# Kernel tuning notes

Hardware: AMD Instinct MI355X
Metric: run time of the kernel (lower is better)

Reference implementation:

```python
import jax, jax.numpy as jnp
import numpy as np

B, CIN, COUT, H, W = 4, 4, 8, 256, 256
FFTH, FFTW = 2 * H - 1, 2 * W - 1  # fftsize = insize + outsize - 1 (padding=True, stride=1)


def setup_inputs() -> dict:
    key = jax.random.key(0)
    k_im, k_w, k_b = jax.random.split(key, 3)
    im = jax.random.normal(k_im, (B, CIN, H, W), dtype=jnp.float32)
    # learned frequency-domain kernel, last dim = (real, imag)
    weight = jax.random.normal(k_w, (COUT, CIN, FFTH, FFTW, 2), dtype=jnp.float32)
    bias = jax.random.normal(k_b, (COUT, 1, 1), dtype=jnp.float32)
    return {"im": im, "weight": weight, "bias": bias}


def reference(im, weight, bias):
    b, cin, h, w = im.shape
    ffth, fftw = 2 * h - 1, 2 * w - 1
    # zero-pad spatially to fftsize; imaginary part is zero (torch pads a trailing complex dim)
    im_p = jnp.pad(im, ((0, 0), (0, 0), (0, ffth - h), (0, fftw - w)))
    f_im = jnp.fft.fft2(im_p.astype(jnp.complex64))              # [B, Cin, fftH, fftW]
    wc = jax.lax.complex(weight[..., 0], weight[..., 1])         # [O, Cin, fftH, fftW]
    # broadcast complex multiply + in-channel reduction fused as a per-frequency contraction;
    # ifft is linear so summing over in-channels before ifft matches the original math
    feats = jnp.einsum('bchw,ochw->bohw', f_im, wc)              # [B, O, fftH, fftW]
    real = jnp.fft.ifft2(feats).real                             # real_feats_mode='index' -> real part
    # crop: cropsize = fftsize - insize = (H-1, W-1); left = floor/2, right = ceil/2
    cl_h, cr_h = (h - 1) // 2, h // 2
    cl_w, cr_w = (w - 1) // 2, w // 2
    real = real[:, :, cl_h:ffth - cr_h, cl_w:fftw - cr_w]        # [B, O, H, W]
    return real + bias                                           # bias [O,1,1] broadcasts
```

## Files before the change

### kernel.cpp

```cpp
#include <hip/hip_runtime.h>
#include <math.h>

#define NN 511
#define HH 256
#define BB 4
#define CINC 4
#define COUTC 8
#define CROP 127
#define INV_NN2 (1.0f / ((float)NN * (float)NN))

typedef _Float16 f16;
typedef _Float16 f16x8 __attribute__((ext_vector_type(8)));
typedef float    f32x4 __attribute__((ext_vector_type(4)));

__device__ __forceinline__ void twid(int a, int b, float& c, float& s) {
    int m = (a * b) % NN;
    float phi = (float)(2.0 * M_PI / (double)NN) * (float)m;
    __sincosf(phi, &s, &c);
}

__global__ void prep_all(const float* __restrict__ im,
                         f16* __restrict__ Aa, f16* __restrict__ Bb,
                         f16* __restrict__ Bd, f16* __restrict__ Ae,
                         f16* __restrict__ imT, f16* __restrict__ feats) {
    int idx = blockIdx.x * 256 + threadIdx.x;
    if (idx < 131072) {
        int m = idx >> 8, y = idx & 255;
        float c, s;
        if (m < 256) { twid(m, y, c, s);       Aa[idx] = (f16)c;    }
        else         { twid(m - 256, y, c, s); Aa[idx] = (f16)(-s); }
    } else if (idx < 655360) {
        int i = idx - 131072;
        int n = i >> 9, k = i & 511;
        float v = 0.f;
        if (n < 2 * NN) {
            int vv = (n < NN) ? n : n - NN;
            int x  = k & 255;
            float c, s; twid(vv, x, c, s);
            if (n < NN) v = (k < 256) ? c : s;
            else        v = (k < 256) ? -s : c;
        }
        Bb[i] = (f16)v;
    } else if (idx < 1179648) {
        int i = idx - 655360;
        int n = i >> 10, k = i & 1023;
        float v = 0.f;
        if (k < 2 * NN) {
            int x  = n & 255;
            int vv = (k < NN) ? k : k - NN;
            float c, s; twid(vv, x + CROP, c, s);
            if (n < 256) v = (k < NN) ? c : -s;
            else         v = (k < NN) ? s : c;
        }
        Bd[i] = (f16)v;
    } else if (idx < 1310720) {
        int i = idx - 1179648;
        int y = i >> 9, k = i & 511;
        float c, s;
        if (k < 256) { twid(k, y + CROP, c, s);       Ae[i] = (f16)c;    }
        else         { twid(k - 256, y + CROP, c, s); Ae[i] = (f16)(-s); }
    } else if (idx < 2359296) {
        int i = idx - 1310720;
        int bc = i >> 16, r = i & 65535;
        int y = r >> 8, x = r & 255;
        imT[(size_t)bc * 65536 + x * 256 + y] = (f16)im[i];
    } else if (idx < 2375680) {
        int i = idx - 2359296;
        feats[(size_t)(i >> 1) * 1024 + 1022 + (i & 1)] = (f16)0.f;
    }
}

__global__ void cmul_h(const f16* __restrict__ F, const float2* __restrict__ W,
                       f16* __restrict__ feats) {
    int idx = blockIdx.x * 256 + threadIdx.x;
    if (idx >= 256 * NN) return;
    int u = idx / NN, v = idx - u * NN;
    int u2 = (u == 0) ? 0 : NN - u;
    int v2 = (v == 0) ? 0 : NN - v;
    float fr[BB][CINC], fi[BB][CINC];
    #pragma unroll
    for (int b = 0; b < BB; ++b)
        #pragma unroll
        for (int c = 0; c < CINC; ++c) {
            size_t row = ((size_t)((b * CINC + c) * 256 + u)) * 1024;
            fr[b][c] = (float)F[row + v];
            fi[b][c] = (float)F[row + NN + v];
        }
    #pragma unroll
    for (int o = 0; o < COUTC; ++o) {
        float whr[CINC], whi[CINC];
        #pragma unroll
        for (int c = 0; c < CINC; ++c) {
            size_t base = (size_t)(o * CINC + c) * NN;
            float2 w1 = W[(base + u)  * NN + v];
            float2 w2 = W[(base + u2) * NN + v2];
            whr[c] = 0.5f * (w1.x + w2.x);
            whi[c] = 0.5f * (w1.y - w2.y);
        }
        #pragma unroll
        for (int b = 0; b < BB; ++b) {
            float hr = 0.f, hi = 0.f;
            #pragma unroll
            for (int c = 0; c < CINC; ++c) {
                hr += fr[b][c] * whr[c] - fi[b][c] * whi[c];
                hi += fr[b][c] * whi[c] + fi[b][c] * whr[c];
            }
            size_t orow = ((size_t)((b * COUTC + o) * 256 + u)) * 1024;
            feats[orow + v]      = (f16)hr;
            feats[orow + NN + v] = (f16)hi;
        }
    }
}

#define GLB_PTR(p) ((const __attribute__((address_space(1))) unsigned int*)(p))
#define LDS_PTR(p) ((__attribute__((address_space(3))) unsigned int*)(p))
__device__ __forceinline__ void gld16(const f16* g, f16* l) {
    __builtin_amdgcn_global_load_lds(GLB_PTR(g), LDS_PTR(l), 16, 0, 0);
}

template<int EPI>
__global__ __launch_bounds__(256)
void gemm128x64(const f16* __restrict__ A, const f16* __restrict__ Bt,
                f16* __restrict__ Ch, float* __restrict__ Cf,
                const float* __restrict__ bias,
                int Kt, int ldA, int ldB, size_t sA, size_t sB) {
    __shared__ __align__(16) f16 As[128 * 64];
    __shared__ __align__(16) f16 Bs[64 * 64];

    const int z  = blockIdx.z;
    const int m0 = blockIdx.x * 128;
    const int n0 = blockIdx.y * 64;
    A  += (size_t)z * sA;
    Bt += (size_t)z * sB;

    const int t    = threadIdx.x;
    const int row  = t >> 3;
    const int slot = t & 7;
    const int kg   = (slot ^ (row & 7)) << 3;
    const f16* Ap = A  + (size_t)(m0 + row) * ldA + kg;
    const f16* Bp = Bt + (size_t)(n0 + row) * ldB + kg;
    f16* lA = As + t * 8;
    f16* lB = Bs + t * 8;

    const int lane = t & 63, w = t >> 6;
    const int wm = (w >> 1) * 64, wn = (w & 1) * 32;
    const int col = lane & 15, quad = lane >> 4;
    const int aswz = col & 7;
    const int offK0 = ((quad)     ^ aswz) << 3;
    const int offK1 = ((4 + quad) ^ aswz) << 3;
    const f16* a_col = As + (wm + col) * 64;
    const f16* b_col = Bs + (wn + col) * 64;

    f32x4 acc[4][2] = {};

    for (int kb = 0; kb < Kt; ++kb) {
        __syncthreads();
        gld16(Ap,             lA);
        gld16(Ap +  32 * ldA, lA + 2048);
        gld16(Ap +  64 * ldA, lA + 4096);
        gld16(Ap +  96 * ldA, lA + 6144);
        gld16(Bp,             lB);
        gld16(Bp +  32 * ldB, lB + 2048);
        Ap += 64; Bp += 64;
        __syncthreads();
        f16x8 af[4][2], bf[2][2];
        #pragma unroll
        for (int i = 0; i < 4; ++i) {
            af[i][0] = *(const f16x8*)(a_col + i * 16 * 64 + offK0);
            af[i][1] = *(const f16x8*)(a_col + i * 16 * 64 + offK1);
        }
        #pragma unroll
        for (int j = 0; j < 2; ++j) {
            bf[j][0] = *(const f16x8*)(b_col + j * 16 * 64 + offK0);
            bf[j][1] = *(const f16x8*)(b_col + j * 16 * 64 + offK1);
        }
        #pragma unroll
        for (int kk = 0; kk < 2; ++kk)
            #pragma unroll
            for (int i = 0; i < 4; ++i)
                #pragma unroll
                for (int j = 0; j < 2; ++j)
                    acc[i][j] = __builtin_amdgcn_mfma_f32_16x16x32_f16(
                        af[i][kk], bf[j][kk], acc[i][j], 0, 0, 0);
    }

    #pragma unroll
    for (int i = 0; i < 4; ++i)
    #pragma unroll
    for (int j = 0; j < 2; ++j) {
        const int mbase = m0 + wm + i * 16 + quad * 4;
        const int ncol  = n0 + wn + j * 16 + col;
        #pragma unroll
        for (int r = 0; r < 4; ++r) {
            const int mm = mbase + r;
            const float val = acc[i][j][r];
            if constexpr (EPI == 0) {
                int u = mm & 255;
                int slotc = (mm < 256) ? ncol : 256 + ncol;
                Ch[((size_t)(z * 256 + u)) * 512 + slotc] = (f16)val;
            } else if constexpr (EPI == 1) {
                Ch[(size_t)mm * 1024 + ncol] = (f16)val;
            } else if constexpr (EPI == 2) {
                int bo = mm >> 8, u = mm & 255;
                int x     = (ncol < 256) ? ncol : ncol - 256;
                int slotc = (ncol < 256) ? u : 256 + u;
                float sc = (u == 0) ? INV_NN2 : 2.f * INV_NN2;
                Ch[((size_t)((bo << 8) + x)) * 512 + slotc] = (f16)(val * sc);
            } else {
                int bo = ncol >> 8, x = ncol & 255;
                Cf[((size_t)bo * 256 + mm) * 256 + x] = val + bias[bo & 7];
            }
        }
    }
}

extern "C" void kernel_launch(void* const* d_in, const int* in_sizes, int n_in,
                              void* d_out, int out_size, void* d_ws, size_t ws_size,
                              hipStream_t stream) {
    const float*  im   = (const float*)d_in[0];
    const float2* W    = (const float2*)d_in[1];
    const float*  bias = (const float*)d_in[2];
    float*        out  = (float*)d_out;

    char* ws = (char*)d_ws;
    f16* Aa    = (f16*)(ws);
    f16* Bb    = (f16*)(ws + 262144);
    f16* Bd    = (f16*)(ws + 1310720);
    f16* Ae    = (f16*)(ws + 2359296);
    f16* imT   = (f16*)(ws + 2621440);
    f16* T1    = (f16*)(ws + 4718592);
    f16* F     = (f16*)(ws + 8912896);
    f16* feats = (f16*)(ws + 17301504);
    f16* T2t   = (f16*)(ws + 34078720);

    prep_all<<<9280, 256, 0, stream>>>(im, Aa, Bb, Bd, Ae, imT, feats);

    gemm128x64<0><<<dim3(4, 4, 16), 256, 0, stream>>>(Aa, imT, T1, nullptr, nullptr,
                                                      4, 256, 256, 0, 65536);
    gemm128x64<1><<<dim3(32, 16, 1), 256, 0, stream>>>(T1, Bb, F, nullptr, nullptr,
                                                       8, 512, 512, 0, 0);
    cmul_h<<<(256 * NN + 255) / 256, 256, 0, stream>>>(F, W, feats);
    gemm128x64<2><<<dim3(64, 8, 1), 256, 0, stream>>>(feats, Bd, T2t, nullptr, nullptr,
                                                      16, 1024, 1024, 0, 0);
    gemm128x64<3><<<dim3(2, 128, 1), 256, 0, stream>>>(Ae, T2t, nullptr, out, bias,
                                                       8, 512, 512, 0, 0);
}
```

Baseline: 170.6 us.

## Fuse second DFT GEMM with complex weight multiply via interleaved layouts

The second row-DFT GEMM and the per-frequency complex multiply / channel reduction are merged into one kernel. The GEMM tile is staged through LDS and the Hermitian-weighted channel contraction is applied directly, so the intermediate F buffer is never written to or re-read from global memory. To make this work, T1 rows are reordered to (u, bc), and Bb and Bd are changed to interleaved real/imag columns, so each tile holds all 16 batch-channel pairs for its frequencies and feats is written as packed half2. The explicit zeroing of feats padding is also dropped. The risk is that the fused epilogue's weight loads and lower parallelism during the multiply phase may limit the gain.

```diff
diff --git a/kernel.cpp b/kernel.cpp
--- a/kernel.cpp
+++ b/kernel.cpp
@@ -10,6 +10,7 @@
 #define INV_NN2 (1.0f / ((float)NN * (float)NN))
 
 typedef _Float16 f16;
+typedef _Float16 f16x2 __attribute__((ext_vector_type(2)));
 typedef _Float16 f16x8 __attribute__((ext_vector_type(8)));
 typedef float    f32x4 __attribute__((ext_vector_type(4)));
 
@@ -22,7 +23,7 @@
 __global__ void prep_all(const float* __restrict__ im,
                          f16* __restrict__ Aa, f16* __restrict__ Bb,
                          f16* __restrict__ Bd, f16* __restrict__ Ae,
-                         f16* __restrict__ imT, f16* __restrict__ feats) {
+                         f16* __restrict__ imT) {
     int idx = blockIdx.x * 256 + threadIdx.x;
     if (idx < 131072) {
         int m = idx >> 8, y = idx & 255;
@@ -32,27 +33,27 @@
     } else if (idx < 655360) {
         int i = idx - 131072;
         int n = i >> 9, k = i & 511;
-        float v = 0.f;
-        if (n < 2 * NN) {
-            int vv = (n < NN) ? n : n - NN;
-            int x  = k & 255;
-            float c, s; twid(vv, x, c, s);
-            if (n < NN) v = (k < 256) ? c : s;
-            else        v = (k < 256) ? -s : c;
-        }
-        Bb[i] = (f16)v;
+        int v = n >> 1, ri = n & 1;
+        float val = 0.f;
+        if (v < NN) {
+            int x = k & 255;
+            float c, s; twid(v, x, c, s);
+            if (ri == 0) val = (k < 256) ? c  : s;
+            else         val = (k < 256) ? -s : c;
+        }
+        Bb[i] = (f16)val;
     } else if (idx < 1179648) {
         int i = idx - 655360;
         int n = i >> 10, k = i & 1023;
-        float v = 0.f;
-        if (k < 2 * NN) {
-            int x  = n & 255;
-            int vv = (k < NN) ? k : k - NN;
-            float c, s; twid(vv, x + CROP, c, s);
-            if (n < 256) v = (k < NN) ? c : -s;
-            else         v = (k < NN) ? s : c;
-        }
-        Bd[i] = (f16)v;
+        int v = k >> 1, ri = k & 1;
+        float val = 0.f;
+        if (v < NN) {
+            int x = n & 255;
+            float c, s; twid(v, x + CROP, c, s);
+            if (ri == 0) val = (n < 256) ? c  : s;
+            else         val = (n < 256) ? -s : c;
+        }
+        Bd[i] = (f16)val;
     } else if (idx < 1310720) {
         int i = idx - 1179648;
         int y = i >> 9, k = i & 511;
@@ -64,51 +65,6 @@
         int bc = i >> 16, r = i & 65535;
         int y = r >> 8, x = r & 255;
         imT[(size_t)bc * 65536 + x * 256 + y] = (f16)im[i];
-    } else if (idx < 2375680) {
-        int i = idx - 2359296;
-        feats[(size_t)(i >> 1) * 1024 + 1022 + (i & 1)] = (f16)0.f;
-    }
-}
-
-__global__ void cmul_h(const f16* __restrict__ F, const float2* __restrict__ W,
-                       f16* __restrict__ feats) {
-    int idx = blockIdx.x * 256 + threadIdx.x;
-    if (idx >= 256 * NN) return;
-    int u = idx / NN, v = idx - u * NN;
-    int u2 = (u == 0) ? 0 : NN - u;
-    int v2 = (v == 0) ? 0 : NN - v;
-    float fr[BB][CINC], fi[BB][CINC];
-    #pragma unroll
-    for (int b = 0; b < BB; ++b)
-        #pragma unroll
-        for (int c = 0; c < CINC; ++c) {
-            size_t row = ((size_t)((b * CINC + c) * 256 + u)) * 1024;
-            fr[b][c] = (float)F[row + v];
-            fi[b][c] = (float)F[row + NN + v];
-        }
-    #pragma unroll
-    for (int o = 0; o < COUTC; ++o) {
-        float whr[CINC], whi[CINC];
-        #pragma unroll
-        for (int c = 0; c < CINC; ++c) {
-            size_t base = (size_t)(o * CINC + c) * NN;
-            float2 w1 = W[(base + u)  * NN + v];
-            float2 w2 = W[(base + u2) * NN + v2];
-            whr[c] = 0.5f * (w1.x + w2.x);
-            whi[c] = 0.5f * (w1.y - w2.y);
-        }
-        #pragma unroll
-        for (int b = 0; b < BB; ++b) {
-            float hr = 0.f, hi = 0.f;
-            #pragma unroll
-            for (int c = 0; c < CINC; ++c) {
-                hr += fr[b][c] * whr[c] - fi[b][c] * whi[c];
-                hi += fr[b][c] * whi[c] + fi[b][c] * whr[c];
-            }
-            size_t orow = ((size_t)((b * COUTC + o) * 256 + u)) * 1024;
-            feats[orow + v]      = (f16)hr;
-            feats[orow + NN + v] = (f16)hi;
-        }
     }
 }
 
@@ -197,9 +153,7 @@
             if constexpr (EPI == 0) {
                 int u = mm & 255;
                 int slotc = (mm < 256) ? ncol : 256 + ncol;
-                Ch[((size_t)(z * 256 + u)) * 512 + slotc] = (f16)val;
-            } else if constexpr (EPI == 1) {
-                Ch[(size_t)mm * 1024 + ncol] = (f16)val;
+                Ch[((size_t)(u * 16 + z)) * 512 + slotc] = (f16)val;
             } else if constexpr (EPI == 2) {
                 int bo = mm >> 8, u = mm & 255;
                 int x     = (ncol < 256) ? ncol : ncol - 256;
@@ -214,6 +168,121 @@
     }
 }
 
+#define LSTR 68
+__global__ __launch_bounds__(256)
+void gemmB_fused(const f16* __restrict__ A, const f16* __restrict__ Bt,
+                 const float2* __restrict__ W, f16* __restrict__ feats) {
+    __shared__ __align__(16) char smem[24576];
+    f16* As = (f16*)smem;
+    f16* Bs = (f16*)(smem + 16384);
+    f16* Ls = (f16*)smem;
+
+    const int m0 = blockIdx.x * 128;
+    const int n0 = blockIdx.y * 64;
+
+    const int t    = threadIdx.x;
+    const int row  = t >> 3;
+    const int slot = t & 7;
+    const int kg   = (slot ^ (row & 7)) << 3;
+    const f16* Ap = A  + (size_t)(m0 + row) * 512 + kg;
+    const f16* Bp = Bt + (size_t)(n0 + row) * 512 + kg;
+    f16* lA = As + t * 8;
+    f16* lB = Bs + t * 8;
+
+    const int lane = t & 63, w = t >> 6;
+    const int wm = (w >> 1) * 64, wn = (w & 1) * 32;
+    const int col = lane & 15, quad = lane >> 4;
+    const int aswz = col & 7;
+    const int offK0 = ((quad)     ^ aswz) << 3;
+    const int offK1 = ((4 + quad) ^ aswz) << 3;
+    const f16* a_col = As + (wm + col) * 64;
+    const f16* b_col = Bs + (wn + col) * 64;
+
+    f32x4 acc[4][2] = {};
+
+    for (int kb = 0; kb < 8; ++kb) {
+        __syncthreads();
+        gld16(Ap,            lA);
+        gld16(Ap + 32 * 512, lA + 2048);
+        gld16(Ap + 64 * 512, lA + 4096);
+        gld16(Ap + 96 * 512, lA + 6144);
+        gld16(Bp,            lB);
+        gld16(Bp + 32 * 512, lB + 2048);
+        Ap += 64; Bp += 64;
+        __syncthreads();
+        f16x8 af[4][2], bf[2][2];
+        #pragma unroll
+        for (int i = 0; i < 4; ++i) {
+            af[i][0] = *(const f16x8*)(a_col + i * 16 * 64 + offK0);
+            af[i][1] = *(const f16x8*)(a_col + i * 16 * 64 + offK1);
+        }
+        #pragma unroll
+        for (int j = 0; j < 2; ++j) {
+            bf[j][0] = *(const f16x8*)(b_col + j * 16 * 64 + offK0);
+            bf[j][1] = *(const f16x8*)(b_col + j * 16 * 64 + offK1);
+        }
+        #pragma unroll
+        for (int kk = 0; kk < 2; ++kk)
+            #pragma unroll
+            for (int i = 0; i < 4; ++i)
+                #pragma unroll
+                for (int j = 0; j < 2; ++j)
+                    acc[i][j] = __builtin_amdgcn_mfma_f32_16x16x32_f16(
+                        af[i][kk], bf[j][kk], acc[i][j], 0, 0, 0);
+    }
+
+    __syncthreads();
+    #pragma unroll
+    for (int i = 0; i < 4; ++i)
+    #pragma unroll
+    for (int j = 0; j < 2; ++j) {
+        const int ml = wm + i * 16 + quad * 4;
+        const int nl = wn + j * 16 + col;
+        #pragma unroll
+        for (int r = 0; r < 4; ++r)
+            Ls[(ml + r) * LSTR + nl] = (f16)acc[i][j][r];
+    }
+    __syncthreads();
+
+    const int du = t >> 5, dv = t & 31;
+    const int u = (m0 >> 4) + du;
+    const int v = (n0 >> 1) + dv;
+    const int u2 = (u == 0) ? 0 : NN - u;
+    const int v2 = (v == 0) ? 0 : NN - v;
+
+    float fr[16], fi[16];
+    #pragma unroll
+    for (int bc = 0; bc < 16; ++bc) {
+        f16x2 p = *(const f16x2*)&Ls[(du * 16 + bc) * LSTR + dv * 2];
+        fr[bc] = (float)p.x;
+        fi[bc] = (float)p.y;
+    }
+
+    #pragma unroll
+    for (int o = 0; o < COUTC; ++o) {
+        float whr[CINC], whi[CINC];
+        #pragma unroll
+        for (int c = 0; c < CINC; ++c) {
+            size_t base = (size_t)(o * CINC + c) * NN;
+            float2 w1 = W[(base + u)  * NN + v];
+            float2 w2 = W[(base + u2) * NN + v2];
+            whr[c] = 0.5f * (w1.x + w2.x);
+            whi[c] = 0.5f * (w1.y - w2.y);
+        }
+        #pragma unroll
+        for (int b = 0; b < BB; ++b) {
+            float hr = 0.f, hi = 0.f;
+            #pragma unroll
+            for (int c = 0; c < CINC; ++c) {
+                hr += fr[b * 4 + c] * whr[c] - fi[b * 4 + c] * whi[c];
+                hi += fr[b * 4 + c] * whi[c] + fi[b * 4 + c] * whr[c];
+            }
+            f16x2 outp; outp.x = (f16)hr; outp.y = (f16)hi;
+            *(f16x2*)&feats[((size_t)((b * COUTC + o) * 256 + u)) * 1024 + v * 2] = outp;
+        }
+    }
+}
+
 extern "C" void kernel_launch(void* const* d_in, const int* in_sizes, int n_in,
                               void* d_out, int out_size, void* d_ws, size_t ws_size,
                               hipStream_t stream) {
@@ -229,17 +298,15 @@
     f16* Ae    = (f16*)(ws + 2359296);
     f16* imT   = (f16*)(ws + 2621440);
     f16* T1    = (f16*)(ws + 4718592);
-    f16* F     = (f16*)(ws + 8912896);
-    f16* feats = (f16*)(ws + 17301504);
-    f16* T2t   = (f16*)(ws + 34078720);
-
-    prep_all<<<9280, 256, 0, stream>>>(im, Aa, Bb, Bd, Ae, imT, feats);
+    f16* feats = (f16*)(ws + 8912896);
+    f16* T2t   = (f16*)(ws + 25690112);
+
+    prep_all<<<9216, 256, 0, stream>>>(im, Aa, Bb, Bd, Ae, imT);
 
     gemm128x64<0><<<dim3(4, 4, 16), 256, 0, stream>>>(Aa, imT, T1, nullptr, nullptr,
                                                       4, 256, 256, 0, 65536);
-    gemm128x64<1><<<dim3(32, 16, 1), 256, 0, stream>>>(T1, Bb, F, nullptr, nullptr,
-                                                       8, 512, 512, 0, 0);
-    cmul_h<<<(256 * NN + 255) / 256, 256, 0, stream>>>(F, W, feats);
+    gemmB_fused<<<dim3(32, 16), 256, 0, stream>>>(T1, Bb, W, feats);
+
     gemm128x64<2><<<dim3(64, 8, 1), 256, 0, stream>>>(feats, Bd, T2t, nullptr, nullptr,
                                                       16, 1024, 1024, 0, 0);
     gemm128x64<3><<<dim3(2, 128, 1), 256, 0, stream>>>(Ae, T2t, nullptr, out, bias,
```

After: 157.3 us. 7.8% less time.
